# Kernel tuning notes

Hardware: AMD Instinct MI355X
Metric: run time of the kernel (lower is better)

The kernel has to match this reference:

```python
import jax, jax.numpy as jnp
import numpy as np
from jax import lax

B, T, D, H, L = 16, 256, 128, 128, 4  # batch, seq, input_size, hidden, num_layers
NUM_CLASSES = 10
EPS = 1e-5


def instancenorm(x):
    # x: [B, T, C]; InstanceNorm1d normalizes over the length dim (T) per (B, C),
    # biased variance, eps=1e-5, no affine.
    m = x.mean(axis=1, keepdims=True)
    v = x.var(axis=1, keepdims=True)
    return (x - m) / jnp.sqrt(v + EPS)


def lstm_stack(x, Wih, Whh, bih, bhh):
    # x: [B, T, I]; Wih/Whh: [L, 4H, I_or_H]; bih/bhh: [L, 4H]. Gate order i,f,g,o.
    batch = x.shape[0]
    hid = Whh.shape[-1]
    out = x
    for l in range(Wih.shape[0]):
        wih, whh, b = Wih[l], Whh[l], bih[l] + bhh[l]
        h0 = jnp.zeros((batch, hid), dtype=x.dtype)
        c0 = jnp.zeros((batch, hid), dtype=x.dtype)
        xs = out.swapaxes(0, 1)  # [T, B, I]

        def step(carry, xt):
            h, c = carry
            g = xt @ wih.T + h @ whh.T + b
            i, f, gg, o = jnp.split(g, 4, axis=-1)
            c_new = jax.nn.sigmoid(f) * c + jax.nn.sigmoid(i) * jnp.tanh(gg)
            h_new = jax.nn.sigmoid(o) * jnp.tanh(c_new)
            return (h_new, c_new), h_new

        _, hs = lax.scan(step, (h0, c0), xs)
        out = hs.swapaxes(0, 1)  # [B, T, H]
    return out


def setup_inputs() -> dict:
    key = jax.random.key(0)
    ks = jax.random.split(key, 16)
    s = 1.0 / np.sqrt(H)
    u = lambda k, shape: jax.random.uniform(k, shape, jnp.float32, -s, s)
    return {
        "x": jax.random.normal(ks[0], (B, T, D), jnp.float32),
        "Wih": u(ks[1], (L, 4 * H, D)),   # input_size == hidden_size so shapes stack
        "Whh": u(ks[2], (L, 4 * H, H)),
        "bih": u(ks[3], (L, 4 * H)),
        "bhh": u(ks[4], (L, 4 * H)),
        "proj_h_w": u(ks[5], (H, H)),
        "proj_h_b": u(ks[6], (H,)),
        "proj_x_w": u(ks[7], (H, D)),
        "proj_x_b": u(ks[8], (H,)),
        "attn_w": u(ks[9], (H,)),
        "fc_w": u(ks[10], (NUM_CLASSES, H)),
        "fc_b": u(ks[11], (NUM_CLASSES,)),
    }


def reference(x, Wih, Whh, bih, bhh, proj_h_w, proj_h_b, proj_x_w, proj_x_b, attn_w, fc_w, fc_b):
    batch, seq_len, input_dim = x.shape
    # normalize(): means/stdev are detached; torch std is unbiased (ddof=1)
    means = lax.stop_gradient(x.mean(axis=(0, 1), keepdims=True))
    stdev = lax.stop_gradient(x.std(axis=(0, 1), ddof=1, keepdims=True) + EPS)
    x = (x - means) / stdev
    x = instancenorm(x)

    lstm_out = lstm_stack(x, Wih, Whh, bih, bhh)   # dropout is identity in eval
    lstm_out = instancenorm(lstm_out)

    ph = lstm_out @ proj_h_w.T + proj_h_b           # [B, T, H]
    px = x @ proj_x_w.T + proj_x_b                  # [B, T, H]
    px = instancenorm(px)

    # additive attention over expanded [B, T, D, H] (values identical across D,
    # matching the original broadcast/expand semantics)
    combined = jnp.tanh(
        jnp.broadcast_to((ph + px)[:, :, None, :], (batch, seq_len, input_dim, ph.shape[-1]))
    )
    logits = jnp.einsum("btdh,h->btd", combined, attn_w)       # [B, T, D]
    alpha = jax.nn.softmax(logits.reshape(batch, -1), axis=1)   # softmax over T*D
    attention_map = alpha.reshape(batch, seq_len, input_dim)

    # classify: context = sum over (T, D) of lstm_out_ex * alpha
    context = jnp.einsum("bth,btd->bh", ph, attention_map)      # [B, H]
    out = context @ fc_w.T + fc_b                               # [B, num_classes]
    return out, attention_map
```

## Files before the change

kernel.cpp:

```cpp
#include <hip/hip_runtime.h>
#include <math.h>
#include <cstddef>

#define B_ 16
#define T_ 256
#define D_ 128
#define H_ 128
#define L_ 4
#define G_ 512
#define NC_ 10
#define EPS_ 1e-5f
#define C_ 16
#define NCHUNK_ (T_ / C_)

#define HROW_ 144
#define HOFF(k) ((k) + (((k) >> 5) << 2))

typedef float f4v __attribute__((ext_vector_type(4)));

#define LOAD_W8(w, base)                                                   \
    asm volatile(                                                          \
        "global_load_dwordx4 %0, %8, off\n\t"                             \
        "global_load_dwordx4 %1, %8, off offset:16\n\t"                   \
        "global_load_dwordx4 %2, %8, off offset:32\n\t"                   \
        "global_load_dwordx4 %3, %8, off offset:48\n\t"                   \
        "global_load_dwordx4 %4, %8, off offset:64\n\t"                   \
        "global_load_dwordx4 %5, %8, off offset:80\n\t"                   \
        "global_load_dwordx4 %6, %8, off offset:96\n\t"                   \
        "global_load_dwordx4 %7, %8, off offset:112\n\t"                  \
        "s_waitcnt vmcnt(0)"                                               \
        : "=&v"(w[0]), "=&v"(w[1]), "=&v"(w[2]), "=&v"(w[3]),              \
          "=&v"(w[4]), "=&v"(w[5]), "=&v"(w[6]), "=&v"(w[7])               \
        : "v"(base)                                                        \
        : "memory")

#define DOT32R(dst_, warr_, hvarr_)                                        \
    {                                                                      \
        float d0_ = 0.f, d1_ = 0.f;                                        \
        _Pragma("unroll")                                                  \
        for (int j_ = 0; j_ < 8; j_++) {                                   \
            d0_ = fmaf(warr_[j_].x, hvarr_[j_].x, d0_);                    \
            d1_ = fmaf(warr_[j_].y, hvarr_[j_].y, d1_);                    \
            d0_ = fmaf(warr_[j_].z, hvarr_[j_].z, d0_);                    \
            d1_ = fmaf(warr_[j_].w, hvarr_[j_].w, d1_);                    \
        }                                                                  \
        dst_ = d0_ + d1_;                                                  \
    }

__device__ __forceinline__ float sigmoid_(float x) {
    x = fminf(fmaxf(x, -30.f), 30.f);
    return 1.f / (1.f + __expf(-x));
}
__device__ __forceinline__ float tanh_(float x) {
    float ax = fminf(fabsf(x), 15.f);
    float e = __expf(2.f * ax);
    float t = 1.f - 2.f / (e + 1.f);
    return copysignf(t, x);
}
__device__ __forceinline__ void wait_ge_(int* p, int v) {
    if (__hip_atomic_load(p, __ATOMIC_RELAXED, __HIP_MEMORY_SCOPE_AGENT) < v) {
        do { __builtin_amdgcn_s_sleep(1); }
        while (__hip_atomic_load(p, __ATOMIC_RELAXED, __HIP_MEMORY_SCOPE_AGENT) < v);
    }
    (void)__hip_atomic_load(p, __ATOMIC_ACQUIRE, __HIP_MEMORY_SCOPE_AGENT);
}
__device__ __forceinline__ void ast_(float* p, float v) {
    __hip_atomic_store(p, v, __ATOMIC_RELAXED, __HIP_MEMORY_SCOPE_AGENT);
}
__device__ __forceinline__ float ald_(const float* p) {
    return __hip_atomic_load(p, __ATOMIC_RELAXED, __HIP_MEMORY_SCOPE_AGENT);
}

#define REC_STEP(RD, WR, PI, PF, PG, PO)                                   \
    {                                                                      \
        const f4v* hb4_ = (const f4v*)(shbuf + (RD) * HROW_ + q * 36);     \
        f4v hv[8];                                                         \
        _Pragma("unroll")                                                  \
        for (int jj_ = 0; jj_ < 8; jj_++) hv[jj_] = hb4_[jj_];             \
        float zi, zf, zg, zo;                                              \
        DOT32R(zi, w0, hv);                                                \
        DOT32R(zf, w1, hv);                                                \
        DOT32R(zg, w2, hv);                                                \
        DOT32R(zo, w3, hv);                                                \
        zi += __shfl_xor(zi, 1); zi += __shfl_xor(zi, 2);                  \
        zf += __shfl_xor(zf, 1); zf += __shfl_xor(zf, 2);                  \
        zg += __shfl_xor(zg, 1); zg += __shfl_xor(zg, 2);                  \
        zo += __shfl_xor(zo, 1); zo += __shfl_xor(zo, 2);                  \
        zi += (PI); zf += (PF); zg += (PG); zo += (PO);                    \
        float ai = sigmoid_(zi), af = sigmoid_(zf);                        \
        float ag = tanh_(zg),    ao = sigmoid_(zo);                        \
        c = fmaf(af, c, ai * ag);                                          \
        float hn = ao * tanh_(c);                                          \
        if (q == 0) {                                                      \
            shbuf[(WR) * HROW_ + HOFF(r)] = hn;                            \
            ast_(hst, hn);                                                 \
        }                                                                  \
        hst += 128;                                                        \
        __syncthreads();                                                   \
    }

__global__ __attribute__((amdgpu_waves_per_eu(2, 2))) __launch_bounds__(512)
void megascan(const float* __restrict__ x,
              const float* __restrict__ Wih, const float* __restrict__ Whh,
              const float* __restrict__ bih, const float* __restrict__ bhh,
              const float* __restrict__ proj_x_w, const float* __restrict__ proj_x_b,
              const float* __restrict__ proj_h_w, const float* __restrict__ proj_h_b,
              const float* __restrict__ attn_w,
              const float* __restrict__ fc_w, const float* __restrict__ fc_b,
              float* __restrict__ mu_bd, float* __restrict__ invn,
              float* __restrict__ psumB, float* __restrict__ psqB,
              float* __restrict__ h_glob,
              float* __restrict__ ring,
              float* __restrict__ px,
              float* __restrict__ mu_px, float* __restrict__ inv_px,
              float* __restrict__ mu_ln, float* __restrict__ inv_ln,
              float* __restrict__ lsc,
              float* __restrict__ out, float* __restrict__ out_att,
              int* __restrict__ flag_h,
              int* __restrict__ flag_g,
              int* __restrict__ flag_px,
              int* __restrict__ flag_ln,
              int* __restrict__ cnt,
              int* __restrict__ flag_norm,
              int* __restrict__ cnt_s) {
    const int wg = blockIdx.x;
    const int tid = threadIdx.x;
    __shared__ __align__(16) float shbuf[16 * HROW_];
    __shared__ __align__(16) float sAs[64][32];
    __shared__ __align__(16) float sBs[32][132];
    __shared__ float sred[64][33];
    __shared__ float stmp[256], swsh[256], sctx[512];
    __shared__ float smu[128], siv[128];

    if (wg < 64) {
        const int r = tid >> 2, q = tid & 3;
        const int l = wg >> 4, b = wg & 15;
        f4v w0[8], w1[8], w2[8], w3[8];
        const float* wl = Whh + (size_t)l * G_ * 128;
        LOAD_W8(w0, wl + ((size_t)(0 * 128 + r)) * 128 + q * 32);
        LOAD_W8(w1, wl + ((size_t)(1 * 128 + r)) * 128 + q * 32);
        LOAD_W8(w2, wl + ((size_t)(2 * 128 + r)) * 128 + q * 32);
        LOAD_W8(w3, wl + ((size_t)(3 * 128 + r)) * 128 + q * 32);
        float c = 0.f;
        if (tid < HROW_) shbuf[tid] = 0.f;
        const float* rsl = ring + ((size_t)l * 16 + b) * (4 * C_ * G_);
        float* hob = h_glob + ((size_t)l * 16 + b) * T_ * 128;
        int* fg = flag_g + l * 16 + b;
        int* fh = flag_h + l * 16 + b;
        __syncthreads();

#pragma unroll 1
        for (int k = 0; k < NCHUNK_; k++) {
            if (tid == 0) wait_ge_(fg, k + 1);
            __syncthreads();
            const float* gb = rsl + (size_t)(k & 3) * C_ * G_;
            float* hst = hob + (size_t)k * C_ * 128 + r;
            float pc0 = ald_(gb + r),                pc1 = ald_(gb + 128 + r);
            float pc2 = ald_(gb + 256 + r),          pc3 = ald_(gb + 384 + r);
            float pc4 = ald_(gb + G_ + r),           pc5 = ald_(gb + G_ + 128 + r);
            float pc6 = ald_(gb + G_ + 256 + r),     pc7 = ald_(gb + G_ + 384 + r);
            float pn0 = ald_(gb + 2 * G_ + r),       pn1 = ald_(gb + 2 * G_ + 128 + r);
            float pn2 = ald_(gb + 2 * G_ + 256 + r), pn3 = ald_(gb + 2 * G_ + 384 + r);
            float pn4 = ald_(gb + 3 * G_ + r),       pn5 = ald_(gb + 3 * G_ + 128 + r);
            float pn6 = ald_(gb + 3 * G_ + 256 + r), pn7 = ald_(gb + 3 * G_ + 384 + r);
#pragma unroll 1
            for (int u = 0; u < 8; u++) {
                float nn0 = 0.f, nn1 = 0.f, nn2 = 0.f, nn3 = 0.f;
                float nn4 = 0.f, nn5 = 0.f, nn6 = 0.f, nn7 = 0.f;
                if (u < 6) {
                    const float* g2 = gb + (size_t)(2 * u + 4) * G_;
                    nn0 = ald_(g2 + r);            nn1 = ald_(g2 + 128 + r);
                    nn2 = ald_(g2 + 256 + r);      nn3 = ald_(g2 + 384 + r);
                    nn4 = ald_(g2 + G_ + r);       nn5 = ald_(g2 + G_ + 128 + r);
                    nn6 = ald_(g2 + G_ + 256 + r); nn7 = ald_(g2 + G_ + 384 + r);
                }
                REC_STEP(0, 1, pc0, pc1, pc2, pc3)
                REC_STEP(1, 0, pc4, pc5, pc6, pc7)
                pc0 = pn0; pc1 = pn1; pc2 = pn2; pc3 = pn3;
                pc4 = pn4; pc5 = pn5; pc6 = pn6; pc7 = pn7;
                pn0 = nn0; pn1 = nn1; pn2 = nn2; pn3 = nn3;
                pn4 = nn4; pn5 = nn5; pn6 = nn6; pn7 = nn7;
            }
            if (tid == 0) __hip_atomic_store(fh, k + 1, __ATOMIC_RELEASE, __HIP_MEMORY_SCOPE_AGENT);
        }
    } else if (wg < 128) {
        const int r = tid >> 2, q = tid & 3;
        const int l = (wg - 64) >> 4, b = (wg - 64) & 15;
        f4v w0[8], w1[8], w2[8], w3[8];
        const float* wl = Wih + (size_t)l * G_ * 128;
        LOAD_W8(w0, wl + ((size_t)(0 * 128 + r)) * 128 + q * 32);
        LOAD_W8(w1, wl + ((size_t)(1 * 128 + r)) * 128 + q * 32);
        LOAD_W8(w2, wl + ((size_t)(2 * 128 + r)) * 128 + q * 32);
        LOAD_W8(w3, wl + ((size_t)(3 * 128 + r)) * 128 + q * 32);
        float bs0 = bih[l * G_ + r] + bhh[l * G_ + r];
        float bs1 = bih[l * G_ + 128 + r] + bhh[l * G_ + 128 + r];
        float bs2 = bih[l * G_ + 256 + r] + bhh[l * G_ + 256 + r];
        float bs3 = bih[l * G_ + 384 + r] + bhh[l * G_ + 384 + r];
        const float* hsrc = (l > 0) ? h_glob + ((size_t)(l - 1) * 16 + b) * T_ * 128
                                    : x + (size_t)b * T_ * 128;
        float muk = 0.f, ivk = 1.f;
        if (l == 0) {
            if (tid == 0) wait_ge_(flag_norm + b, 1);
            __syncthreads();
            muk = mu_bd[b * 128 + (tid & 127)];
            ivk = invn[b * 128 + (tid & 127)];
        }
        float* rout = ring + ((size_t)l * 16 + b) * (4 * C_ * G_);
        int* fhp = (l > 0) ? flag_h + (l - 1) * 16 + b : flag_h;
        int* fhme = flag_h + l * 16 + b;
        int* fgo = flag_g + l * 16 + b;

#pragma unroll 1
        for (int k = 0; k < NCHUNK_; k++) {
            if (tid == 0) {
                if (l > 0) wait_ge_(fhp, k + 1);
                if (k >= 4) wait_ge_(fhme, k - 3);
            }
            __syncthreads();
#pragma unroll
            for (int i = 0; i < 4; i++) {
                int idx = i * 512 + tid;
                float v;
                if (l == 0) {
                    v = hsrc[(size_t)k * C_ * 128 + idx];
                    v = (v - muk) * ivk;
                } else {
                    v = ald_(hsrc + (size_t)k * C_ * 128 + idx);
                }
                shbuf[(idx >> 7) * HROW_ + HOFF(idx & 127)] = v;
            }
            __syncthreads();
#pragma unroll 4
            for (int s = 0; s < C_; s++) {
                const f4v* hb4 = (const f4v*)(shbuf + s * HROW_ + q * 36);
                f4v hv[8];
#pragma unroll
                for (int j = 0; j < 8; j++) hv[j] = hb4[j];
                float z0, z1, z2, z3;
                DOT32R(z0, w0, hv);
                DOT32R(z1, w1, hv);
                DOT32R(z2, w2, hv);
                DOT32R(z3, w3, hv);
                z0 += __shfl_xor(z0, 1); z0 += __shfl_xor(z0, 2);
                z1 += __shfl_xor(z1, 1); z1 += __shfl_xor(z1, 2);
                z2 += __shfl_xor(z2, 1); z2 += __shfl_xor(z2, 2);
                z3 += __shfl_xor(z3, 1); z3 += __shfl_xor(z3, 2);
                if (q == 0) {
                    float* ro = rout + ((size_t)(k & 3) * C_ + s) * G_;
                    ast_(ro + r, z0 + bs0);
                    ast_(ro + 128 + r, z1 + bs1);
                    ast_(ro + 256 + r, z2 + bs2);
                    ast_(ro + 384 + r, z3 + bs3);
                }
            }
            __syncthreads();
            if (tid == 0) __hip_atomic_store(fgo, k + 1, __ATOMIC_RELEASE, __HIP_MEMORY_SCOPE_AGENT);
        }
    } else if (wg < 144) {
        const int b = wg - 128;
        const int h = tid & 127, tq = tid >> 7;
        f4v w0[8], w1[8], w2[8], w3[8];
        LOAD_W8(w0, proj_x_w + (size_t)h * 128 + 0);
        LOAD_W8(w1, proj_x_w + (size_t)h * 128 + 32);
        LOAD_W8(w2, proj_x_w + (size_t)h * 128 + 64);
        LOAD_W8(w3, proj_x_w + (size_t)h * 128 + 96);
        float bsx = proj_x_b[h];
        if (tid == 0) wait_ge_(flag_norm + b, 1);
        __syncthreads();
        float muk = mu_bd[b * 128 + h], ivk = invn[b * 128 + h];
        const float* xb = x + (size_t)b * T_ * 128;
        float* pxb = px + (size_t)b * T_ * 128;
        float sacc = 0.f, qacc = 0.f;

        for (int blk = 0; blk < 16; blk++) {
            int t0 = blk * 16;
            __syncthreads();
#pragma unroll
            for (int j = 0; j < 4; j++) {
                int tt = tq * 4 + j;
                float v = xb[(size_t)(t0 + tt) * 128 + h];
                shbuf[tt * HROW_ + HOFF(h)] = (v - muk) * ivk;
            }
            __syncthreads();
#pragma unroll
            for (int j = 0; j < 4; j++) {
                int tt = tq * 4 + j;
                const float* row = shbuf + tt * HROW_;
                f4v hv[8];
                float p0, p1, p2, p3;
                const f4v* r4 = (const f4v*)(row + 0 * 36);
#pragma unroll
                for (int u = 0; u < 8; u++) hv[u] = r4[u];
                DOT32R(p0, w0, hv);
                r4 = (const f4v*)(row + 1 * 36);
#pragma unroll
                for (int u = 0; u < 8; u++) hv[u] = r4[u];
                DOT32R(p1, w1, hv);
                r4 = (const f4v*)(row + 2 * 36);
#pragma unroll
                for (int u = 0; u < 8; u++) hv[u] = r4[u];
                DOT32R(p2, w2, hv);
                r4 = (const f4v*)(row + 3 * 36);
#pragma unroll
                for (int u = 0; u < 8; u++) hv[u] = r4[u];
                DOT32R(p3, w3, hv);
                float val = (p0 + p1) + (p2 + p3) + bsx;
                ast_(pxb + (size_t)(t0 + tt) * 128 + h, val);
                sacc += val; qacc += val * val;
            }
        }
        __syncthreads();
        shbuf[tq * 128 + h] = sacc;
        shbuf[512 + tq * 128 + h] = qacc;
        __syncthreads();
        if (tq == 0) {
            float s = shbuf[h] + shbuf[128 + h] + shbuf[256 + h] + shbuf[384 + h];
            float qq = shbuf[512 + h] + shbuf[640 + h] + shbuf[768 + h] + shbuf[896 + h];
            float m = s * (1.f / T_);
            float v = qq * (1.f / T_) - m * m;
            ast_(mu_px + b * 128 + h, m);
            ast_(inv_px + b * 128 + h, rsqrtf(fmaxf(v, 0.f) + EPS_));
        }
        __syncthreads();
        if (tid == 0) __hip_atomic_store(flag_px + b, 1, __ATOMIC_RELEASE, __HIP_MEMORY_SCOPE_AGENT);
    } else if (wg < 160) {
        const int b = wg - 144;
        const int h = tid & 127, st = tid >> 7;
        const float* hsrc = h_glob + ((size_t)3 * 16 + b) * T_ * 128;
        int* f3 = flag_h + 3 * 16 + b;
        float s = 0.f, q = 0.f;
        for (int k = 0; k < NCHUNK_; k++) {
            if (tid == 0) wait_ge_(f3, k + 1);
            __syncthreads();
#pragma unroll
            for (int j = 0; j < 4; j++) {
                int tt = st * 4 + j;
                float v = ald_(hsrc + (size_t)(k * C_ + tt) * 128 + h);
                s += v; q += v * v;
            }
        }
        shbuf[st * 128 + h] = s;
        shbuf[512 + st * 128 + h] = q;
        __syncthreads();
        if (st == 0) {
            float ss = shbuf[h] + shbuf[128 + h] + shbuf[256 + h] + shbuf[384 + h];
            float qq = shbuf[512 + h] + shbuf[640 + h] + shbuf[768 + h] + shbuf[896 + h];
            float m = ss * (1.f / T_);
            float v = qq * (1.f / T_) - m * m;
            ast_(mu_ln + b * 128 + h, m);
            ast_(inv_ln + b * 128 + h, rsqrtf(fmaxf(v, 0.f) + EPS_));
        }
        __syncthreads();
        if (tid == 0) __hip_atomic_store(flag_ln + b, 1, __ATOMIC_RELEASE, __HIP_MEMORY_SCOPE_AGENT);
    } else if (wg < 224) {
        const int blk = wg - 160;
        const int b = blk >> 2, qt = blk & 3;
        const int m0 = qt * 64;
        if (tid == 0) { wait_ge_(flag_px + b, 1); wait_ge_(flag_ln + b, 1); }
        __syncthreads();
        if (tid < 128) {
            smu[tid] = mu_px[b * 128 + tid];
            siv[tid] = inv_px[b * 128 + tid];
        }
        __syncthreads();

        const float* h3b = h_glob + ((size_t)3 * 16 + b) * T_ * 128;
        float* phg = h_glob;
        const int lr = tid >> 3, lc = (tid & 7) << 2;
        const int nB = tid >> 2, k0B = (tid & 3) << 3;
        const int tm = (tid >> 5) << 2, tn = (tid & 31) << 2;
        float acc[4][4] = {};
        const float* mup = mu_ln + b * 128;
        const float* ivp = inv_ln + b * 128;
        for (int kb = 0; kb < 128; kb += 32) {
            float4 av = *(const float4*)(h3b + (size_t)(m0 + lr) * 128 + kb + lc);
            float4 m4 = *(const float4*)(mup + kb + lc);
            float4 i4 = *(const float4*)(ivp + kb + lc);
            av.x = (av.x - m4.x) * i4.x; av.y = (av.y - m4.y) * i4.y;
            av.z = (av.z - m4.z) * i4.z; av.w = (av.w - m4.w) * i4.w;
            float4 bv0 = *(const float4*)(proj_h_w + (size_t)nB * 128 + kb + k0B);
            float4 bv1 = *(const float4*)(proj_h_w + (size_t)nB * 128 + kb + k0B + 4);
            __syncthreads();
            *(float4*)&sAs[lr][lc] = av;
            sBs[k0B + 0][nB] = bv0.x; sBs[k0B + 1][nB] = bv0.y;
            sBs[k0B + 2][nB] = bv0.z; sBs[k0B + 3][nB] = bv0.w;
            sBs[k0B + 4][nB] = bv1.x; sBs[k0B + 5][nB] = bv1.y;
            sBs[k0B + 6][nB] = bv1.z; sBs[k0B + 7][nB] = bv1.w;
            __syncthreads();
#pragma unroll
            for (int k4 = 0; k4 < 8; k4++) {
                f4v a4[4];
#pragma unroll
                for (int i = 0; i < 4; i++) a4[i] = *(const f4v*)&sAs[tm + i][k4 * 4];
#pragma unroll
                for (int kk = 0; kk < 4; kk++) {
                    f4v b4 = *(const f4v*)&sBs[k4 * 4 + kk][tn];
#pragma unroll
                    for (int i = 0; i < 4; i++) {
                        acc[i][0] = fmaf(a4[i][kk], b4.x, acc[i][0]);
                        acc[i][1] = fmaf(a4[i][kk], b4.y, acc[i][1]);
                        acc[i][2] = fmaf(a4[i][kk], b4.z, acc[i][2]);
                        acc[i][3] = fmaf(a4[i][kk], b4.w, acc[i][3]);
                    }
                }
            }
        }
        float spart[4];
#pragma unroll
        for (int i = 0; i < 4; i++) {
            int t = m0 + tm + i;
            size_t prow = ((size_t)b * 256 + t) * 128;
            f4v pxv = *(const f4v*)(px + prow + tn);
            float sp = 0.f;
#pragma unroll
            for (int j = 0; j < 4; j++) {
                int col = tn + j;
                float val = acc[i][j] + proj_h_b[col];
                ast_(phg + prow + col, val);
                float inx = (pxv[j] - smu[col]) * siv[col];
                sp = fmaf(tanh_(val + inx), attn_w[col], sp);
            }
            spart[i] = sp;
        }
        __syncthreads();
#pragma unroll
        for (int i = 0; i < 4; i++) sred[tm + i][tid & 31] = spart[i];
        __syncthreads();
        if (tid < 64) {
            float s = 0.f;
#pragma unroll
            for (int j = 0; j < 32; j++) s += sred[tid][j];
            ast_(lsc + b * 256 + m0 + tid, s);
        }
        __syncthreads();
        if (tid == 0) {
            (void)__hip_atomic_fetch_add(cnt + b, 1, __ATOMIC_ACQ_REL, __HIP_MEMORY_SCOPE_AGENT);
            wait_ge_(cnt + b, 4);
        }
        __syncthreads();
        float v = 0.f;
        if (tid < 256) { v = lsc[b * 256 + tid]; stmp[tid] = v; }
        __syncthreads();
        for (int off = 128; off > 0; off >>= 1) {
            if (tid < off) stmp[tid] = fmaxf(stmp[tid], stmp[tid + off]);
            __syncthreads();
        }
        float mx = stmp[0];
        __syncthreads();
        float e = (tid < 256) ? __expf(v - mx) : 0.f;
        if (tid < 256) stmp[tid] = e;
        __syncthreads();
        for (int off = 128; off > 0; off >>= 1) {
            if (tid < off) stmp[tid] += stmp[tid + off];
            __syncthreads();
        }
        float tot = stmp[0];
        __syncthreads();
        if (tid < 256) swsh[tid] = e / tot;
        __syncthreads();
        {
            float* ob = out_att + (size_t)b * T_ * D_ + (size_t)m0 * 128;
            const float invD = 1.f / (float)D_;
            for (int i = tid; i < 64 * 128; i += 512)
                ob[i] = swsh[m0 + (i >> 7)] * invD;
        }
        if (qt == 0) {
            int h = tid & 127, st = tid >> 7;
            float a = 0.f;
            for (int tt = st * 64; tt < st * 64 + 64; tt++)
                a = fmaf(phg[((size_t)b * 256 + tt) * 128 + h], swsh[tt], a);
            sctx[st * 128 + h] = a;
            __syncthreads();
            if (tid < 128) sctx[tid] = sctx[tid] + sctx[128 + tid] + sctx[256 + tid] + sctx[384 + tid];
            __syncthreads();
            if (tid < NC_) {
                float s = fc_b[tid];
                const float* fw = fc_w + tid * 128;
                for (int k = 0; k < 128; k++) s = fmaf(sctx[k], fw[k], s);
                out[b * NC_ + tid] = s;
            }
        }
    } else {
        const int b = wg - 224;
        const int d = tid & 127, r = tid >> 7;
        const float* xb = x + (size_t)b * T_ * 128;
        float s = 0.f, q = 0.f;
        for (int t = r; t < T_; t += 4) {
            float v = xb[(size_t)t * 128 + d];
            s += v; q += v * v;
        }
        shbuf[tid] = s; shbuf[512 + tid] = q;
        __syncthreads();
        if (r == 0) {
            s = shbuf[d] + shbuf[128 + d] + shbuf[256 + d] + shbuf[384 + d];
            q = shbuf[512 + d] + shbuf[640 + d] + shbuf[768 + d] + shbuf[896 + d];
            ast_(psumB + b * 128 + d, s);
            ast_(psqB + b * 128 + d, q);
        }
        __syncthreads();
        if (tid == 0) {
            (void)__hip_atomic_fetch_add(cnt_s, 1, __ATOMIC_ACQ_REL, __HIP_MEMORY_SCOPE_AGENT);
            wait_ge_(cnt_s, 16);
        }
        __syncthreads();
        if (tid < 128) {
            float S = 0.f, Q = 0.f, sb = 0.f, qb = 0.f;
            for (int bb = 0; bb < 16; bb++) {
                float ps = psumB[bb * 128 + tid];
                float pq = psqB[bb * 128 + tid];
                S += ps; Q += pq;
                if (bb == b) { sb = ps; qb = pq; }
            }
            float n = (float)(B_ * T_);
            float m = S / n;
            float varu = (Q - n * m * m) / (n - 1.f);
            float sd = sqrtf(fmaxf(varu, 0.f)) + EPS_;
            float mu = sb * (1.f / T_);
            float varT = qb * (1.f / T_) - mu * mu;
            ast_(mu_bd + b * 128 + tid, mu);
            ast_(invn + b * 128 + tid, rsqrtf(fmaxf(varT, 0.f) + EPS_ * sd * sd));
        }
        __syncthreads();
        if (tid == 0) __hip_atomic_store(flag_norm + b, 1, __ATOMIC_RELEASE, __HIP_MEMORY_SCOPE_AGENT);
    }
}

extern "C" void kernel_launch(void* const* d_in, const int* in_sizes, int n_in,
                              void* d_out, int out_size, void* d_ws, size_t ws_size,
                              hipStream_t stream) {
    const float* x        = (const float*)d_in[0];
    const float* Wih      = (const float*)d_in[1];
    const float* Whh      = (const float*)d_in[2];
    const float* bih      = (const float*)d_in[3];
    const float* bhh      = (const float*)d_in[4];
    const float* proj_h_w = (const float*)d_in[5];
    const float* proj_h_b = (const float*)d_in[6];
    const float* proj_x_w = (const float*)d_in[7];
    const float* proj_x_b = (const float*)d_in[8];
    const float* attn_w   = (const float*)d_in[9];
    const float* fc_w     = (const float*)d_in[10];
    const float* fc_b     = (const float*)d_in[11];
    float* out = (float*)d_out;

    float* ws = (float*)d_ws;
    const size_t NTD = (size_t)B_ * T_ * D_;
    float* h_glob = ws;
    float* ring   = h_glob + 4 * NTD;
    float* px     = ring + 4 * NTD;
    float* smalls = px + NTD;
    float* psumB  = smalls;
    float* psqB   = psumB + 2048;
    float* mu_bd  = psqB + 2048;
    float* invn   = mu_bd + 2048;
    float* mu_ln  = invn + 2048;
    float* inv_ln = mu_ln + 2048;
    float* mu_px  = inv_ln + 2048;
    float* inv_px = mu_px + 2048;
    float* lsc    = inv_px + 2048;
    int*   flags  = (int*)(lsc + 4096);
    int*   flag_h   = flags;
    int*   flag_g   = flags + 64;
    int*   flag_px  = flags + 128;
    int*   flag_ln  = flags + 144;
    int*   cnt      = flags + 160;
    int*   flag_norm= flags + 176;
    int*   cnt_s    = flags + 192;

    hipMemsetAsync((void*)flags, 0, 256 * sizeof(int), stream);

    megascan<<<240, 512, 0, stream>>>(x, Wih, Whh, bih, bhh,
                                      proj_x_w, proj_x_b, proj_h_w, proj_h_b,
                                      attn_w, fc_w, fc_b,
                                      mu_bd, invn, psumB, psqB,
                                      h_glob, ring, px,
                                      mu_px, inv_px, mu_ln, inv_ln,
                                      lsc, out, out + B_ * NC_,
                                      flag_h, flag_g, flag_px, flag_ln, cnt,
                                      flag_norm, cnt_s);
}
```

Measured before the change: 462.7 us.

## Process two batch recurrences per recurrent workgroup to halve barrier count

Result: slower. 744.2 us (+60.8%).

```diff
diff --git a/kernel.cpp b/kernel.cpp
--- a/kernel.cpp
+++ b/kernel.cpp
@@ -71,9 +71,17 @@
     return __hip_atomic_load(p, __ATOMIC_RELAXED, __HIP_MEMORY_SCOPE_AGENT);
 }
 
-#define REC_STEP(RD, WR, PI, PF, PG, PO)                                   \
+#define RING_LD8(dst_, gp_)                                                \
     {                                                                      \
-        const f4v* hb4_ = (const f4v*)(shbuf + (RD) * HROW_ + q * 36);     \
+        dst_[0] = ald_((gp_) + r);            dst_[1] = ald_((gp_) + 128 + r); \
+        dst_[2] = ald_((gp_) + 256 + r);      dst_[3] = ald_((gp_) + 384 + r); \
+        dst_[4] = ald_((gp_) + G_ + r);       dst_[5] = ald_((gp_) + G_ + 128 + r); \
+        dst_[6] = ald_((gp_) + G_ + 256 + r); dst_[7] = ald_((gp_) + G_ + 384 + r); \
+    }
+
+#define REC_STEP2(SB, RD, WR, PI, PF, PG, PO, CC, HST)                     \
+    {                                                                      \
+        const f4v* hb4_ = (const f4v*)(shbuf + ((SB) * 2 + (RD)) * HROW_ + q * 36); \
         f4v hv[8];                                                         \
         _Pragma("unroll")                                                  \
         for (int jj_ = 0; jj_ < 8; jj_++) hv[jj_] = hb4_[jj_];             \
@@ -89,14 +97,13 @@
         zi += (PI); zf += (PF); zg += (PG); zo += (PO);                    \
         float ai = sigmoid_(zi), af = sigmoid_(zf);                        \
         float ag = tanh_(zg),    ao = sigmoid_(zo);                        \
-        c = fmaf(af, c, ai * ag);                                          \
-        float hn = ao * tanh_(c);                                          \
+        CC = fmaf(af, CC, ai * ag);                                        \
+        float hn = ao * tanh_(CC);                                         \
         if (q == 0) {                                                      \
-            shbuf[(WR) * HROW_ + HOFF(r)] = hn;                            \
-            ast_(hst, hn);                                                 \
+            shbuf[((SB) * 2 + (WR)) * HROW_ + HOFF(r)] = hn;               \
+            ast_((HST), hn);                                               \
         }                                                                  \
-        hst += 128;                                                        \
-        __syncthreads();                                                   \
+        (HST) += 128;                                                      \
     }
 
 __global__ __attribute__((amdgpu_waves_per_eu(2, 2))) __launch_bounds__(512)
@@ -132,60 +139,71 @@
     __shared__ float stmp[256], swsh[256], sctx[512];
     __shared__ float smu[128], siv[128];
 
-    if (wg < 64) {
+    if (wg < 32) {
         const int r = tid >> 2, q = tid & 3;
-        const int l = wg >> 4, b = wg & 15;
+        const int l = wg >> 3, p = wg & 7;
+        const int b0 = p * 2, b1 = p * 2 + 1;
         f4v w0[8], w1[8], w2[8], w3[8];
         const float* wl = Whh + (size_t)l * G_ * 128;
         LOAD_W8(w0, wl + ((size_t)(0 * 128 + r)) * 128 + q * 32);
         LOAD_W8(w1, wl + ((size_t)(1 * 128 + r)) * 128 + q * 32);
         LOAD_W8(w2, wl + ((size_t)(2 * 128 + r)) * 128 + q * 32);
         LOAD_W8(w3, wl + ((size_t)(3 * 128 + r)) * 128 + q * 32);
-        float c = 0.f;
-        if (tid < HROW_) shbuf[tid] = 0.f;
-        const float* rsl = ring + ((size_t)l * 16 + b) * (4 * C_ * G_);
-        float* hob = h_glob + ((size_t)l * 16 + b) * T_ * 128;
-        int* fg = flag_g + l * 16 + b;
-        int* fh = flag_h + l * 16 + b;
+        float cA = 0.f, cB = 0.f;
+        if (tid < 288) { shbuf[tid] = 0.f; shbuf[288 + tid] = 0.f; }
+        const float* rsA = ring + ((size_t)l * 16 + b0) * (4 * C_ * G_);
+        const float* rsB = ring + ((size_t)l * 16 + b1) * (4 * C_ * G_);
+        float* hoA = h_glob + ((size_t)l * 16 + b0) * T_ * 128;
+        float* hoB = h_glob + ((size_t)l * 16 + b1) * T_ * 128;
+        int* fgA = flag_g + l * 16 + b0;
+        int* fgB = flag_g + l * 16 + b1;
+        int* fhA = flag_h + l * 16 + b0;
+        int* fhB = flag_h + l * 16 + b1;
         __syncthreads();
 
 #pragma unroll 1
         for (int k = 0; k < NCHUNK_; k++) {
-            if (tid == 0) wait_ge_(fg, k + 1);
-            __syncthreads();
-            const float* gb = rsl + (size_t)(k & 3) * C_ * G_;
-            float* hst = hob + (size_t)k * C_ * 128 + r;
-            float pc0 = ald_(gb + r),                pc1 = ald_(gb + 128 + r);
-            float pc2 = ald_(gb + 256 + r),          pc3 = ald_(gb + 384 + r);
-            float pc4 = ald_(gb + G_ + r),           pc5 = ald_(gb + G_ + 128 + r);
-            float pc6 = ald_(gb + G_ + 256 + r),     pc7 = ald_(gb + G_ + 384 + r);
-            float pn0 = ald_(gb + 2 * G_ + r),       pn1 = ald_(gb + 2 * G_ + 128 + r);
-            float pn2 = ald_(gb + 2 * G_ + 256 + r), pn3 = ald_(gb + 2 * G_ + 384 + r);
-            float pn4 = ald_(gb + 3 * G_ + r),       pn5 = ald_(gb + 3 * G_ + 128 + r);
-            float pn6 = ald_(gb + 3 * G_ + 256 + r), pn7 = ald_(gb + 3 * G_ + 384 + r);
+            if (tid == 0) { wait_ge_(fgA, k + 1); wait_ge_(fgB, k + 1); }
+            __syncthreads();
+            const float* gA = rsA + (size_t)(k & 3) * C_ * G_;
+            const float* gB = rsB + (size_t)(k & 3) * C_ * G_;
+            float* hsA = hoA + (size_t)k * C_ * 128 + r;
+            float* hsB = hoB + (size_t)k * C_ * 128 + r;
+            float pcA[8], pnA[8], pcB[8], pnB[8];
+            RING_LD8(pcA, gA);
+            RING_LD8(pcB, gB);
+            RING_LD8(pnA, gA + 2 * G_);
+            RING_LD8(pnB, gB + 2 * G_);
 #pragma unroll 1
             for (int u = 0; u < 8; u++) {
-                float nn0 = 0.f, nn1 = 0.f, nn2 = 0.f, nn3 = 0.f;
-                float nn4 = 0.f, nn5 = 0.f, nn6 = 0.f, nn7 = 0.f;
+                float nnA[8], nnB[8];
                 if (u < 6) {
-                    const float* g2 = gb + (size_t)(2 * u + 4) * G_;
-                    nn0 = ald_(g2 + r);            nn1 = ald_(g2 + 128 + r);
-                    nn2 = ald_(g2 + 256 + r);      nn3 = ald_(g2 + 384 + r);
-                    nn4 = ald_(g2 + G_ + r);       nn5 = ald_(g2 + G_ + 128 + r);
-                    nn6 = ald_(g2 + G_ + 256 + r); nn7 = ald_(g2 + G_ + 384 + r);
+                    RING_LD8(nnA, gA + (size_t)(2 * u + 4) * G_);
+                    RING_LD8(nnB, gB + (size_t)(2 * u + 4) * G_);
+                } else {
+#pragma unroll
+                    for (int j = 0; j < 8; j++) { nnA[j] = 0.f; nnB[j] = 0.f; }
                 }
-                REC_STEP(0, 1, pc0, pc1, pc2, pc3)
-                REC_STEP(1, 0, pc4, pc5, pc6, pc7)
-                pc0 = pn0; pc1 = pn1; pc2 = pn2; pc3 = pn3;
-                pc4 = pn4; pc5 = pn5; pc6 = pn6; pc7 = pn7;
-                pn0 = nn0; pn1 = nn1; pn2 = nn2; pn3 = nn3;
-                pn4 = nn4; pn5 = nn5; pn6 = nn6; pn7 = nn7;
-            }
-            if (tid == 0) __hip_atomic_store(fh, k + 1, __ATOMIC_RELEASE, __HIP_MEMORY_SCOPE_AGENT);
-        }
-    } else if (wg < 128) {
+                REC_STEP2(0, 0, 1, pcA[0], pcA[1], pcA[2], pcA[3], cA, hsA)
+                REC_STEP2(1, 0, 1, pcB[0], pcB[1], pcB[2], pcB[3], cB, hsB)
+                __syncthreads();
+                REC_STEP2(0, 1, 0, pcA[4], pcA[5], pcA[6], pcA[7], cA, hsA)
+                REC_STEP2(1, 1, 0, pcB[4], pcB[5], pcB[6], pcB[7], cB, hsB)
+#pragma unroll
+                for (int j = 0; j < 8; j++) {
+                    pcA[j] = pnA[j]; pnA[j] = nnA[j];
+                    pcB[j] = pnB[j]; pnB[j] = nnB[j];
+                }
+                __syncthreads();
+            }
+            if (tid == 0) {
+                __hip_atomic_store(fhA, k + 1, __ATOMIC_RELEASE, __HIP_MEMORY_SCOPE_AGENT);
+                __hip_atomic_store(fhB, k + 1, __ATOMIC_RELEASE, __HIP_MEMORY_SCOPE_AGENT);
+            }
+        }
+    } else if (wg < 96) {
         const int r = tid >> 2, q = tid & 3;
-        const int l = (wg - 64) >> 4, b = (wg - 64) & 15;
+        const int l = (wg - 32) >> 4, b = (wg - 32) & 15;
         f4v w0[8], w1[8], w2[8], w3[8];
         const float* wl = Wih + (size_t)l * G_ * 128;
         LOAD_W8(w0, wl + ((size_t)(0 * 128 + r)) * 128 + q * 32);
@@ -256,8 +274,8 @@
             __syncthreads();
             if (tid == 0) __hip_atomic_store(fgo, k + 1, __ATOMIC_RELEASE, __HIP_MEMORY_SCOPE_AGENT);
         }
-    } else if (wg < 144) {
-        const int b = wg - 128;
+    } else if (wg < 112) {
+        const int b = wg - 96;
         const int h = tid & 127, tq = tid >> 7;
         f4v w0[8], w1[8], w2[8], w3[8];
         LOAD_W8(w0, proj_x_w + (size_t)h * 128 + 0);
@@ -323,8 +341,8 @@
         }
         __syncthreads();
         if (tid == 0) __hip_atomic_store(flag_px + b, 1, __ATOMIC_RELEASE, __HIP_MEMORY_SCOPE_AGENT);
-    } else if (wg < 160) {
-        const int b = wg - 144;
+    } else if (wg < 128) {
+        const int b = wg - 112;
         const int h = tid & 127, st = tid >> 7;
         const float* hsrc = h_glob + ((size_t)3 * 16 + b) * T_ * 128;
         int* f3 = flag_h + 3 * 16 + b;
@@ -352,8 +370,8 @@
         }
         __syncthreads();
         if (tid == 0) __hip_atomic_store(flag_ln + b, 1, __ATOMIC_RELEASE, __HIP_MEMORY_SCOPE_AGENT);
-    } else if (wg < 224) {
-        const int blk = wg - 160;
+    } else if (wg < 192) {
+        const int blk = wg - 128;
         const int b = blk >> 2, qt = blk & 3;
         const int m0 = qt * 64;
         if (tid == 0) { wait_ge_(flag_px + b, 1); wait_ge_(flag_ln + b, 1); }
@@ -481,7 +499,7 @@
             }
         }
     } else {
-        const int b = wg - 224;
+        const int b = wg - 192;
         const int d = tid & 127, r = tid >> 7;
         const float* xb = x + (size_t)b * T_ * 128;
         float s = 0.f, q = 0.f;
@@ -568,7 +586,7 @@
 
     hipMemsetAsync((void*)flags, 0, 256 * sizeof(int), stream);
 
-    megascan<<<240, 512, 0, stream>>>(x, Wih, Whh, bih, bhh,
+    megascan<<<208, 512, 0, stream>>>(x, Wih, Whh, bih, bhh,
                                       proj_x_w, proj_x_b, proj_h_w, proj_h_b,
                                       attn_w, fc_w, fc_b,
                                       mu_bd, invn, psumB, psqB,
```
